# Kernel optimization log

Measured on AMD Instinct MI355X. Metric: run time of the kernel, lower is better.

The kernel has to match this reference:

```python
import jax, jax.numpy as jnp
import numpy as np

N_HEADS = 12


def setup_inputs() -> dict:
    key = jax.random.key(0)
    k1, k2, k3 = jax.random.split(key, 3)
    B, W, C = 2, 2048, 768
    in_sequence_bwc = jax.random.normal(k1, (B, W, C), dtype=jnp.float32)
    # QKV projection weight [3C, C] (torch Linear convention: out_features x in_features)
    w_attn = jax.random.normal(k2, (3 * C, C), dtype=jnp.float32) * (1.0 / np.sqrt(C))
    w_proj = jax.random.normal(k3, (C, C), dtype=jnp.float32) * (1.0 / np.sqrt(C))
    return {"in_sequence_bwc": in_sequence_bwc, "w_attn": w_attn, "w_proj": w_proj}


def reference(in_sequence_bwc, w_attn, w_proj):
    B, W, C = in_sequence_bwc.shape
    H = N_HEADS
    K = C // H  # head dim
    qkv = jnp.einsum('bwc,dc->bwd', in_sequence_bwc, w_attn)  # [B,W,3C]
    q, k, v = jnp.split(qkv, 3, axis=-1)
    # [B,H,W,K]
    q = q.reshape(B, W, H, K).transpose(0, 2, 1, 3)
    k = k.reshape(B, W, H, K).transpose(0, 2, 1, 3)
    v = v.reshape(B, W, H, K).transpose(0, 2, 1, 3)
    scores = jnp.einsum('bhqk,bhsk->bhqs', q, k) / jnp.sqrt(jnp.float32(K))
    causal = jnp.tril(jnp.ones((W, W), dtype=bool))
    scores = jnp.where(causal[None, None], scores, jnp.float32(-jnp.inf))
    probs = jax.nn.softmax(scores, axis=-1)
    out = jnp.einsum('bhqs,bhsk->bhqk', probs, v)  # [B,H,W,K]
    out = out.transpose(0, 2, 1, 3).reshape(B, W, C)
    return jnp.einsum('bwc,dc->bwd', out, w_proj)
```

## Files before the change

### kernel.cpp

```cpp
#include <hip/hip_runtime.h>

constexpr int B_  = 2;
constexpr int W_  = 2048;
constexpr int C_  = 768;
constexpr int H_  = 12;
constexpr int HD  = 64;
constexpr int C3  = 3 * C_;
constexpr int M_  = B_ * W_;
constexpr int NSLOT = 72;

typedef float  f32x4 __attribute__((ext_vector_type(4)));
typedef short  s16x8 __attribute__((ext_vector_type(8)));
typedef short  s16x4 __attribute__((ext_vector_type(4)));
typedef unsigned short u16;
typedef unsigned int   u32;

__device__ __forceinline__ u16 f2bf(float f) {
    unsigned int u = __float_as_uint(f);
    u += 0x7FFFu + ((u >> 16) & 1u);
    return (u16)(u >> 16);
}
__device__ __forceinline__ float bf2f(u16 v) {
    return __uint_as_float(((u32)v) << 16);
}

__device__ __forceinline__ void gload_lds16(const u16* g, u16* l) {
    __builtin_amdgcn_global_load_lds(
        (const __attribute__((address_space(1))) unsigned int*)g,
        (__attribute__((address_space(3))) unsigned int*)l, 16, 0, 0);
}

__global__ __launch_bounds__(256)
void cvt_all(const float* __restrict__ x, const float* __restrict__ wa,
             const float* __restrict__ wp, u16* __restrict__ xb,
             u16* __restrict__ wab, u16* __restrict__ wpb)
{
    const int n0 = M_ * C_ / 8;
    const int n1 = n0 + C3 * C_ / 8;
    const int n2 = n1 + C_ * C_ / 8;
    int i = blockIdx.x * 256 + threadIdx.x;
    const float* s; u16* d; int j;
    if (i < n0)      { s = x;  d = xb;  j = i; }
    else if (i < n1) { s = wa; d = wab; j = i - n0; }
    else if (i < n2) { s = wp; d = wpb; j = i - n1; }
    else return;
    const float4 a = reinterpret_cast<const float4*>(s)[j * 2];
    const float4 b = reinterpret_cast<const float4*>(s)[j * 2 + 1];
    s16x8 v;
    v[0] = (short)f2bf(a.x); v[1] = (short)f2bf(a.y);
    v[2] = (short)f2bf(a.z); v[3] = (short)f2bf(a.w);
    v[4] = (short)f2bf(b.x); v[5] = (short)f2bf(b.y);
    v[6] = (short)f2bf(b.z); v[7] = (short)f2bf(b.w);
    reinterpret_cast<s16x8*>(d)[j] = v;
}

__device__ __forceinline__ void store_out(u16*  p, float v) { *p = f2bf(v); }
__device__ __forceinline__ void store_out(float* p, float v) { *p = v; }

template <typename OutT>
__global__ __launch_bounds__(256)
void gemm_nt_mfma(const u16* __restrict__ A, const u16* __restrict__ Bm,
                  OutT* __restrict__ Y, int Ndim, int Kdim)
{
    __shared__ __align__(16) u16 As[3][128 * 32];
    __shared__ __align__(16) u16 Bs[3][128 * 32];

    const int t  = threadIdx.x;
    const int w  = t >> 6;
    const int l  = t & 63;
    const int lg = l >> 4;
    const int ln = l & 15;
    const int wm = w >> 1;
    const int wn = w & 1;
    const int m0 = blockIdx.x * 128;
    const int n0 = blockIdx.y * 128;

    f32x4 acc[4][4];
    #pragma unroll
    for (int mi = 0; mi < 4; ++mi)
        #pragma unroll
        for (int ni = 0; ni < 4; ++ni)
            acc[mi][ni] = (f32x4){0.f, 0.f, 0.f, 0.f};

    size_t off[2];
    #pragma unroll
    for (int it = 0; it < 2; ++it) {
        const int c  = t + it * 256;
        off[it] = (size_t)((c >> 6) * 16 + (c & 15)) * Kdim + ((c >> 4) & 3) * 8;
    }

    #define GEMM_STAGE(buf, k0s)                                              \
        _Pragma("unroll")                                                     \
        for (int it = 0; it < 2; ++it) {                                      \
            gload_lds16(A  + (size_t)m0 * Kdim + (k0s) + off[it],             \
                        &As[buf][(size_t)(it * 256 + w * 64) * 8]);           \
            gload_lds16(Bm + (size_t)n0 * Kdim + (k0s) + off[it],             \
                        &Bs[buf][(size_t)(it * 256 + w * 64) * 8]);           \
        }

    GEMM_STAGE(0, 0)
    GEMM_STAGE(1, 32)

    int cur = 0;
    for (int k0 = 0; k0 < Kdim; k0 += 32) {
        if (k0 + 32 < Kdim)
            asm volatile("s_waitcnt vmcnt(4)" ::: "memory");
        else
            asm volatile("s_waitcnt vmcnt(0)" ::: "memory");
        __builtin_amdgcn_s_barrier();

        const int nx2 = (cur + 2 >= 3) ? cur - 1 : cur + 2;
        if (k0 + 64 < Kdim) { GEMM_STAGE(nx2, k0 + 64) }

        s16x8 af[4], bf[4];
        #pragma unroll
        for (int mi = 0; mi < 4; ++mi)
            af[mi] = *reinterpret_cast<const s16x8*>(
                &As[cur][(size_t)((wm * 4 + mi) * 64 + l) * 8]);
        #pragma unroll
        for (int ni = 0; ni < 4; ++ni)
            bf[ni] = *reinterpret_cast<const s16x8*>(
                &Bs[cur][(size_t)((wn * 4 + ni) * 64 + l) * 8]);
        #pragma unroll
        for (int mi = 0; mi < 4; ++mi)
            #pragma unroll
            for (int ni = 0; ni < 4; ++ni)
                acc[mi][ni] = __builtin_amdgcn_mfma_f32_16x16x32_bf16(
                    af[mi], bf[ni], acc[mi][ni], 0, 0, 0);

        cur = (cur == 2) ? 0 : cur + 1;
    }
    #undef GEMM_STAGE

    #pragma unroll
    for (int mi = 0; mi < 4; ++mi) {
        const int row = m0 + wm * 64 + mi * 16 + lg * 4;
        #pragma unroll
        for (int ni = 0; ni < 4; ++ni) {
            const int col = n0 + wn * 64 + ni * 16 + ln;
            #pragma unroll
            for (int r = 0; r < 4; ++r)
                store_out(&Y[(size_t)(row + r) * Ndim + col], acc[mi][ni][r]);
        }
    }
}

__global__ __launch_bounds__(256)
void attn_partial(const u16* __restrict__ qkv, u16* __restrict__ po,
                  float* __restrict__ pl)
{
    __shared__ __align__(16) unsigned char KsB[64 * 128];
    __shared__ __align__(16) unsigned char VtB[64 * 144];

    const int t  = threadIdx.x;
    const int w  = t >> 6;
    const int l  = t & 63;
    const int lg = l >> 4;
    const int ln = l & 15;
    const int p  = (NSLOT - 1) - (int)blockIdx.x;
    const int h  = blockIdx.y;
    const int b  = blockIdx.z;

    int qt = 0, cumv = 0;
    while (cumv + ((qt >> 1) + 1) <= p) { cumv += (qt >> 1) + 1; ++qt; }
    const int ck = p - cumv;

    const int qb  = qt * 128;
    const int q0w = qb + w * 32;
    const int g0  = ck * 4;
    const int g1  = min(2 * (qt + 1), g0 + 4);
    const int slot = (b * H_ + h) * NSLOT + p;

    const u16* base  = qkv + (size_t)(b * W_) * C3;
    const u16* kbase = base + C_ + h * HD;
    const u16* vbase = base + 2 * C_ + h * HD;

    s16x8 qf[2][2];
    #pragma unroll
    for (int m = 0; m < 2; ++m) {
        const u16* qrow = base + (size_t)(q0w + m * 16 + ln) * C3 + h * HD;
        #pragma unroll
        for (int kc = 0; kc < 2; ++kc)
            qf[m][kc] = *reinterpret_cast<const s16x8*>(&qrow[kc * 32 + lg * 8]);
    }

    s16x8 onesf;
    {
        const short v1 = (ln == 0) ? (short)0x3F80 : (short)0;
        #pragma unroll
        for (int i = 0; i < 8; ++i) onesf[i] = v1;
    }

    f32x4 o[2][4];
    #pragma unroll
    for (int m = 0; m < 2; ++m)
        #pragma unroll
        for (int i = 0; i < 4; ++i) o[m][i] = (f32x4){0.f, 0.f, 0.f, 0.f};
    f32x4 o4[2] = { (f32x4){0.f,0.f,0.f,0.f}, (f32x4){0.f,0.f,0.f,0.f} };

    const float c1 = 0.18033688011112042f;
    const float c2 = 17.312340490667562f;

    const size_t sk_off = (size_t)((t >> 7) * 16 + (t & 15)) * C3
                        + ((t >> 6) & 1) * 32 + ((t >> 4) & 3) * 8;
    const bool vstage = (t < 128);
    const int vrun = (t >> 4) & 7;
    const int vK0  = (vrun >> 2) * 32 + (vrun & 3) * 4;
    const int vdq  = (t & 15) * 4;
    const int kfb  = l * 16;

    s16x8 kr[2];
    s16x4 vr[8];

    {
        const int s0 = g0 * 64;
        const u16* ks = kbase + (size_t)s0 * C3 + sk_off;
        kr[0] = *reinterpret_cast<const s16x8*>(ks);
        kr[1] = *reinterpret_cast<const s16x8*>(ks + (size_t)32 * C3);
        if (vstage) {
            const u16* vsrc = vbase + (size_t)(s0 + vK0) * C3 + vdq;
            #pragma unroll
            for (int e = 0; e < 8; ++e)
                vr[e] = *reinterpret_cast<const s16x4*>(
                    &vsrc[(size_t)((e >> 2) * 16 + (e & 3)) * C3]);
        }
    }

    for (int g = g0; g < g1; ++g) {
        const int s0 = g * 64;

        __syncthreads();

        *reinterpret_cast<s16x8*>(KsB + t * 16)         = kr[0];
        *reinterpret_cast<s16x8*>(KsB + (t + 256) * 16) = kr[1];
        if (vstage) {
            #pragma unroll
            for (int j = 0; j < 4; ++j) {
                s16x8 pk = { vr[0][j], vr[1][j], vr[2][j], vr[3][j],
                             vr[4][j], vr[5][j], vr[6][j], vr[7][j] };
                *reinterpret_cast<s16x8*>(
                    VtB + (vdq + j) * 144 + vrun * 16) = pk;
            }
        }

        if (g + 1 < g1) {
            const int s1 = s0 + 64;
            const u16* ks = kbase + (size_t)s1 * C3 + sk_off;
            kr[0] = *reinterpret_cast<const s16x8*>(ks);
            kr[1] = *reinterpret_cast<const s16x8*>(ks + (size_t)32 * C3);
            if (vstage) {
                const u16* vsrc = vbase + (size_t)(s1 + vK0) * C3 + vdq;
                #pragma unroll
                for (int e = 0; e < 8; ++e)
                    vr[e] = *reinterpret_cast<const s16x4*>(
                        &vsrc[(size_t)((e >> 2) * 16 + (e & 3)) * C3]);
            }
        }

        __syncthreads();

        #pragma unroll
        for (int c = 0; c < 2; ++c) {
            if (s0 + c * 32 <= q0w + 31) {
                const bool act0 = (s0 + c * 32 <= q0w + 15);
                float pt[2][2][4];
                #pragma unroll
                for (int n2 = 0; n2 < 2; ++n2) {
                    const unsigned char* kfrag = KsB + (c * 2 + n2) * 2048 + kfb;
                    s16x8 kf0 = *reinterpret_cast<const s16x8*>(kfrag);
                    s16x8 kf1 = *reinterpret_cast<const s16x8*>(kfrag + 1024);
                    #pragma unroll
                    for (int m = 0; m < 2; ++m) {
                        if (m == 1 || act0) {
                            f32x4 s = (f32x4){0.f, 0.f, 0.f, 0.f};
                            __builtin_amdgcn_s_setprio(1);
                            s = __builtin_amdgcn_mfma_f32_16x16x32_bf16(
                                kf0, qf[m][0], s, 0, 0, 0);
                            s = __builtin_amdgcn_mfma_f32_16x16x32_bf16(
                                kf1, qf[m][1], s, 0, 0, 0);
                            __builtin_amdgcn_s_setprio(0);
                            const int kg0   = s0 + c * 32 + n2 * 16 + lg * 4;
                            const int klast = s0 + c * 32 + n2 * 16 + 15;
                            const int qbase = q0w + m * 16;
                            if (klast <= qbase) {
                                #pragma unroll
                                for (int r = 0; r < 4; ++r)
                                    pt[m][n2][r] = exp2f(fmaf(s[r], c1, -c2));
                            } else {
                                const int qg = qbase + ln;
                                #pragma unroll
                                for (int r = 0; r < 4; ++r)
                                    pt[m][n2][r] = (kg0 + r <= qg)
                                              ? exp2f(fmaf(s[r], c1, -c2)) : 0.0f;
                            }
                        }
                    }
                }
                s16x8 vf[4];
                #pragma unroll
                for (int dt = 0; dt < 4; ++dt)
                    vf[dt] = *reinterpret_cast<const s16x8*>(
                        VtB + (dt * 16 + ln) * 144 + c * 64 + lg * 16);
                #pragma unroll
                for (int m = 0; m < 2; ++m) {
                    if (m == 1 || act0) {
                        union { s16x8 v; u32 wd[4]; } afu;
                        asm("v_cvt_pk_bf16_f32 %0, %1, %2"
                            : "=v"(afu.wd[0]) : "v"(pt[m][0][0]), "v"(pt[m][0][1]));
                        asm("v_cvt_pk_bf16_f32 %0, %1, %2"
                            : "=v"(afu.wd[1]) : "v"(pt[m][0][2]), "v"(pt[m][0][3]));
                        asm("v_cvt_pk_bf16_f32 %0, %1, %2"
                            : "=v"(afu.wd[2]) : "v"(pt[m][1][0]), "v"(pt[m][1][1]));
                        asm("v_cvt_pk_bf16_f32 %0, %1, %2"
                            : "=v"(afu.wd[3]) : "v"(pt[m][1][2]), "v"(pt[m][1][3]));
                        const s16x8 af = afu.v;
                        __builtin_amdgcn_s_setprio(1);
                        #pragma unroll
                        for (int dt = 0; dt < 4; ++dt)
                            o[m][dt] = __builtin_amdgcn_mfma_f32_16x16x32_bf16(
                                af, vf[dt], o[m][dt], 0, 0, 0);
                        o4[m] = __builtin_amdgcn_mfma_f32_16x16x32_bf16(
                            af, onesf, o4[m], 0, 0, 0);
                        __builtin_amdgcn_s_setprio(0);
                    }
                }
            }
        }
    }

    #pragma unroll
    for (int m = 0; m < 2; ++m) {
        if (ln == 0) {
            #pragma unroll
            for (int r = 0; r < 4; ++r)
                pl[(size_t)slot * 128 + w * 32 + m * 16 + lg * 4 + r] = o4[m][r];
        }
        u16* os = po + (size_t)slot * 8192;
        #pragma unroll
        for (int r = 0; r < 4; ++r)
            #pragma unroll
            for (int dt = 0; dt < 4; ++dt)
                os[(w * 32 + m * 16 + lg * 4 + r) * 64 + dt * 16 + ln] =
                    f2bf(o[m][dt][r]);
    }
}

__global__ __launch_bounds__(256)
void attn_combine(const u16* __restrict__ po, const float* __restrict__ pl,
                  u16* __restrict__ aob)
{
    const int qt = blockIdx.x >> 2;
    const int rg = blockIdx.x & 3;
    const int h  = blockIdx.y;
    const int b  = blockIdx.z;
    const int a  = qt >> 1;
    const int nc = a + 1;
    const int cum = (qt & 1) ? (a + 1) * (a + 1) : a * (a + 1);
    const int slot0 = (b * H_ + h) * NSLOT + cum;

    const int tid = threadIdx.x;
    const int i   = rg * 32 + (tid >> 3);
    const int d0  = (tid & 7) * 8;

    float acc[8] = {};
    float lt = 0.0f;
    for (int c = 0; c < nc; ++c) {
        const u16* os = po + (size_t)(slot0 + c) * 8192 + i * 64 + d0;
        s16x8 vv = *reinterpret_cast<const s16x8*>(os);
        #pragma unroll
        for (int e = 0; e < 8; ++e) acc[e] += bf2f((u16)vv[e]);
        lt += pl[(size_t)(slot0 + c) * 128 + i];
    }
    const float inv = 1.0f / lt;

    u16* dst = aob + (size_t)(b * W_ + qt * 128 + i) * C_ + h * HD + d0;
    s16x8 ov;
    #pragma unroll
    for (int e = 0; e < 8; ++e) ov[e] = (short)f2bf(acc[e] * inv);
    *reinterpret_cast<s16x8*>(dst) = ov;
}

extern "C" void kernel_launch(void* const* d_in, const int* in_sizes, int n_in,
                              void* d_out, int out_size, void* d_ws, size_t ws_size,
                              hipStream_t stream)
{
    const float* x      = (const float*)d_in[0];
    const float* w_attn = (const float*)d_in[1];
    const float* w_proj = (const float*)d_in[2];
    float* out = (float*)d_out;

    u16* xb   = (u16*)d_ws;
    u16* wab  = xb   + (size_t)M_ * C_;
    u16* wpb  = wab  + (size_t)C3 * C_;
    u16* qkvb = wpb  + (size_t)C_ * C_;
    u16* aob  = qkvb + (size_t)M_ * C3;
    u16* po   = aob  + (size_t)M_ * C_;
    float* pl = (float*)(po + (size_t)B_ * H_ * NSLOT * 8192);

    {
        const int total8 = (M_ * C_ + C3 * C_ + C_ * C_) / 8;
        cvt_all<<<(total8 + 255) / 256, 256, 0, stream>>>(
            x, w_attn, w_proj, xb, wab, wpb);
    }

    {
        dim3 grid(M_ / 128, C3 / 128);
        gemm_nt_mfma<u16><<<grid, 256, 0, stream>>>(xb, wab, qkvb, C3, C_);
    }

    {
        dim3 grid(NSLOT, H_, B_);
        attn_partial<<<grid, 256, 0, stream>>>(qkvb, po, pl);
    }
    {
        dim3 grid((W_ / 128) * 4, H_, B_);
        attn_combine<<<grid, 256, 0, stream>>>(po, pl, aob);
    }

    {
        dim3 grid(M_ / 128, C_ / 128);
        gemm_nt_mfma<float><<<grid, 256, 0, stream>>>(aob, wpb, out, C_, C_);
    }
}
```

Measured before the change: 114.0 us.

## Template GEMM on M tile size and switch to double-buffered LDS pipeline

The GEMM kernel is templated on the M tile height, and the output projection now uses 64-row tiles, doubling its grid from 192 to 384 blocks so more of the GPU's compute units have work. The LDS pipeline also changes from a triple-buffered scheme with explicit vmcnt waits to a simpler double buffer with __syncthreads around each k-step. This lowers LDS use and may raise occupancy, but prefetch now waits for all loads each iteration, so less memory latency is hidden, which could slow the larger QKV GEMM.

```diff
diff --git a/kernel.cpp b/kernel.cpp
--- a/kernel.cpp
+++ b/kernel.cpp
@@ -57,13 +57,15 @@
 __device__ __forceinline__ void store_out(u16*  p, float v) { *p = f2bf(v); }
 __device__ __forceinline__ void store_out(float* p, float v) { *p = v; }
 
-template <typename OutT>
+template <int BM, typename OutT>
 __global__ __launch_bounds__(256)
 void gemm_nt_mfma(const u16* __restrict__ A, const u16* __restrict__ Bm,
                   OutT* __restrict__ Y, int Ndim, int Kdim)
 {
-    __shared__ __align__(16) u16 As[3][128 * 32];
-    __shared__ __align__(16) u16 Bs[3][128 * 32];
+    constexpr int MF  = BM / 32;
+    constexpr int AIT = BM / 64;
+    __shared__ __align__(16) u16 As[2][BM * 32];
+    __shared__ __align__(16) u16 Bs[2][128 * 32];
 
     const int t  = threadIdx.x;
     const int w  = t >> 6;
@@ -72,12 +74,12 @@
     const int ln = l & 15;
     const int wm = w >> 1;
     const int wn = w & 1;
-    const int m0 = blockIdx.x * 128;
+    const int m0 = blockIdx.x * BM;
     const int n0 = blockIdx.y * 128;
 
-    f32x4 acc[4][4];
-    #pragma unroll
-    for (int mi = 0; mi < 4; ++mi)
+    f32x4 acc[MF][4];
+    #pragma unroll
+    for (int mi = 0; mi < MF; ++mi)
         #pragma unroll
         for (int ni = 0; ni < 4; ++ni)
             acc[mi][ni] = (f32x4){0.f, 0.f, 0.f, 0.f};
@@ -91,50 +93,45 @@
 
     #define GEMM_STAGE(buf, k0s)                                              \
         _Pragma("unroll")                                                     \
-        for (int it = 0; it < 2; ++it) {                                      \
+        for (int it = 0; it < AIT; ++it)                                      \
             gload_lds16(A  + (size_t)m0 * Kdim + (k0s) + off[it],             \
                         &As[buf][(size_t)(it * 256 + w * 64) * 8]);           \
+        _Pragma("unroll")                                                     \
+        for (int it = 0; it < 2; ++it)                                        \
             gload_lds16(Bm + (size_t)n0 * Kdim + (k0s) + off[it],             \
-                        &Bs[buf][(size_t)(it * 256 + w * 64) * 8]);           \
-        }
+                        &Bs[buf][(size_t)(it * 256 + w * 64) * 8]);
 
     GEMM_STAGE(0, 0)
-    GEMM_STAGE(1, 32)
+    __syncthreads();
 
     int cur = 0;
     for (int k0 = 0; k0 < Kdim; k0 += 32) {
-        if (k0 + 32 < Kdim)
-            asm volatile("s_waitcnt vmcnt(4)" ::: "memory");
-        else
-            asm volatile("s_waitcnt vmcnt(0)" ::: "memory");
-        __builtin_amdgcn_s_barrier();
-
-        const int nx2 = (cur + 2 >= 3) ? cur - 1 : cur + 2;
-        if (k0 + 64 < Kdim) { GEMM_STAGE(nx2, k0 + 64) }
-
-        s16x8 af[4], bf[4];
-        #pragma unroll
-        for (int mi = 0; mi < 4; ++mi)
+        if (k0 + 32 < Kdim) { GEMM_STAGE(cur ^ 1, k0 + 32) }
+
+        s16x8 af[MF], bf[4];
+        #pragma unroll
+        for (int mi = 0; mi < MF; ++mi)
             af[mi] = *reinterpret_cast<const s16x8*>(
-                &As[cur][(size_t)((wm * 4 + mi) * 64 + l) * 8]);
+                &As[cur][(size_t)((wm * MF + mi) * 64 + l) * 8]);
         #pragma unroll
         for (int ni = 0; ni < 4; ++ni)
             bf[ni] = *reinterpret_cast<const s16x8*>(
                 &Bs[cur][(size_t)((wn * 4 + ni) * 64 + l) * 8]);
         #pragma unroll
-        for (int mi = 0; mi < 4; ++mi)
+        for (int mi = 0; mi < MF; ++mi)
             #pragma unroll
             for (int ni = 0; ni < 4; ++ni)
                 acc[mi][ni] = __builtin_amdgcn_mfma_f32_16x16x32_bf16(
                     af[mi], bf[ni], acc[mi][ni], 0, 0, 0);
 
-        cur = (cur == 2) ? 0 : cur + 1;
+        __syncthreads();
+        cur ^= 1;
     }
     #undef GEMM_STAGE
 
     #pragma unroll
-    for (int mi = 0; mi < 4; ++mi) {
-        const int row = m0 + wm * 64 + mi * 16 + lg * 4;
+    for (int mi = 0; mi < MF; ++mi) {
+        const int row = m0 + wm * (MF * 16) + mi * 16 + lg * 4;
         #pragma unroll
         for (int ni = 0; ni < 4; ++ni) {
             const int col = n0 + wn * 64 + ni * 16 + ln;
@@ -405,7 +402,7 @@
 
     {
         dim3 grid(M_ / 128, C3 / 128);
-        gemm_nt_mfma<u16><<<grid, 256, 0, stream>>>(xb, wab, qkvb, C3, C_);
+        gemm_nt_mfma<128, u16><<<grid, 256, 0, stream>>>(xb, wab, qkvb, C3, C_);
     }
 
     {
@@ -418,7 +415,7 @@
     }
 
     {
-        dim3 grid(M_ / 128, C_ / 128);
-        gemm_nt_mfma<float><<<grid, 256, 0, stream>>>(aob, wpb, out, C_, C_);
-    }
-}
+        dim3 grid(M_ / 64, C_ / 128);
+        gemm_nt_mfma<64, float><<<grid, 256, 0, stream>>>(aob, wpb, out, C_, C_);
+    }
+}
```

Measured after the change: 109.9 us. -3.6%, faster.
